# Kernel tuning notes

Measured on AMD Instinct MI355X. Metric: run time of the kernel, lower is better.

## Reference

```python
import jax, jax.numpy as jnp
import numpy as np

ROPE_BASE = 10000.0

def apply_rope(x, offset=0):
    # x: [B, H, L, Dh], traditional (interleaved-pair) RoPE
    B, H, L, Dh = x.shape
    pos = jnp.arange(L, dtype=jnp.float32) + offset            # [L]
    freqs = ROPE_BASE ** (-jnp.arange(0, Dh, 2, dtype=jnp.float32) / Dh)  # [Dh/2]
    theta = pos[:, None] * freqs[None, :]                      # [L, Dh/2]
    cos, sin = jnp.cos(theta), jnp.sin(theta)
    x1 = x[..., 0::2]                                          # [B,H,L,Dh/2]
    x2 = x[..., 1::2]
    r1 = x1 * cos - x2 * sin
    r2 = x1 * sin + x2 * cos
    return jnp.stack([r1, r2], axis=-1).reshape(B, H, L, Dh)


def setup_inputs() -> dict:
    key = jax.random.key(0)
    ks = jax.random.split(key, 5)
    B, L, D = 2, 2048, 2048
    s = 1.0 / np.sqrt(D)
    x = jax.random.normal(ks[0], (B, L, D), dtype=jnp.float32)
    # additive causal mask (0 on/below diagonal, -1e9 above)
    mask = jnp.where(jnp.tril(jnp.ones((L, L), dtype=bool)), 0.0, -1e9).astype(jnp.float32)
    Wq = jax.random.normal(ks[1], (D, D), dtype=jnp.float32) * s
    Wk = jax.random.normal(ks[2], (D, D), dtype=jnp.float32) * s
    Wv = jax.random.normal(ks[3], (D, D), dtype=jnp.float32) * s
    Wo = jax.random.normal(ks[4], (D, D), dtype=jnp.float32) * s
    return {"x": x, "mask": mask, "Wq": Wq, "Wk": Wk, "Wv": Wv, "Wo": Wo}


def reference(x, mask, Wq, Wk, Wv, Wo):
    num_heads = 16
    B, L, D = x.shape
    Dh = D // num_heads
    q = (x @ Wq.T).reshape(B, L, num_heads, Dh).transpose(0, 2, 1, 3)  # [B,H,L,Dh]
    k = (x @ Wk.T).reshape(B, L, num_heads, Dh).transpose(0, 2, 1, 3)
    v = (x @ Wv.T).reshape(B, L, num_heads, Dh).transpose(0, 2, 1, 3)
    q = apply_rope(q)
    k = apply_rope(k)
    scale = 1.0 / jnp.sqrt(jnp.float32(Dh))
    scores = jnp.einsum('bhqd,bhkd->bhqk', q * scale, k) + mask  # [B,H,L,L]
    probs = jax.nn.softmax(scores, axis=-1)
    vh = jnp.einsum('bhqk,bhkd->bhqd', probs, v)                 # [B,H,L,Dh]
    vh = vh.transpose(0, 2, 1, 3).reshape(B, L, D)
    out = vh @ Wo.T
    return out, k, v
```

## Files before the change

### kernel.cpp

```cpp
#include <hip/hip_runtime.h>

typedef __attribute__((ext_vector_type(4))) float f32x4;
typedef __attribute__((ext_vector_type(8))) __bf16 bf16x8;

__device__ __forceinline__ unsigned short f2b(float f) {
  unsigned int u = __builtin_bit_cast(unsigned int, f);
  u = (u + 0x7fffu + ((u >> 16) & 1u)) >> 16;
  return (unsigned short)u;
}
__device__ __forceinline__ float b2f(unsigned short h) {
  unsigned int u = ((unsigned int)h) << 16;
  return __builtin_bit_cast(float, u);
}
__device__ __forceinline__ void gl_lds16(const void* g, void* l) {
  __builtin_amdgcn_global_load_lds(
      (const __attribute__((address_space(1))) void*)g,
      (__attribute__((address_space(3))) void*)l, 16, 0, 0);
}

__global__ void prep_kernel(const float* __restrict__ x, unsigned short* __restrict__ xb,
                            const float* __restrict__ s0, const float* __restrict__ s1,
                            const float* __restrict__ s2, const float* __restrict__ s3,
                            unsigned short* __restrict__ d0, unsigned short* __restrict__ d1,
                            unsigned short* __restrict__ d2, unsigned short* __restrict__ d3,
                            float2* __restrict__ tab) {
  int z = blockIdx.y;
  int i = blockIdx.x * blockDim.x + threadIdx.x;
  if (z == 5) {
    if (i >= 131072) return;
    int l = i >> 6, k = i & 63;
    float freq = __builtin_amdgcn_exp2f(-(float)(2 * k) * (13.287712379549449f / 128.0f));
    float th = (float)l * freq;
    tab[i] = make_float2(cosf(th), sinf(th));
    return;
  }
  const float* src; unsigned short* dst; int n4;
  if (z == 0)      { src = x;  dst = xb; n4 = 2097152; }
  else if (z == 1) { src = s0; dst = d0; n4 = 1048576; }
  else if (z == 2) { src = s1; dst = d1; n4 = 1048576; }
  else if (z == 3) { src = s2; dst = d2; n4 = 1048576; }
  else             { src = s3; dst = d3; n4 = 1048576; }
  if (i >= n4) return;
  float4 v = ((const float4*)src)[i];
  ushort4 o;
  o.x = f2b(v.x); o.y = f2b(v.y); o.z = f2b(v.z); o.w = f2b(v.w);
  ((ushort4*)dst)[i] = o;
}

__global__ __launch_bounds__(256) void fix_kernel(unsigned short* __restrict__ qb,
                                                  unsigned short* __restrict__ kb,
                                                  float* __restrict__ kout,
                                                  const unsigned short* __restrict__ vb,
                                                  unsigned short* __restrict__ vt,
                                                  float* __restrict__ vout,
                                                  const float2* __restrict__ tab) {
  __shared__ unsigned short t[32][33];
  const float QS = 0.12751743f;
  int z = blockIdx.y;
  if (z == 2) {
    int bid = blockIdx.x;
    if (bid >= 8192) return;
    int lx = bid & 63, dy = (bid >> 6) & 3, bz = bid >> 8;
    int b = bz >> 4, h = bz & 15;
    int l0 = lx * 32, d0 = dy * 32;
    const unsigned short* src = vb + (size_t)b * 2048 * 2048 + h * 128;
    unsigned short* dst = vt + (size_t)bz * 128 * 2048;
    int tx = threadIdx.x & 31, ty = threadIdx.x >> 5;
#pragma unroll
    for (int i = 0; i < 4; ++i) {
      unsigned short u = src[(size_t)(l0 + ty + 8 * i) * 2048 + d0 + tx];
      t[ty + 8 * i][tx] = u;
      vout[((size_t)bz * 2048 + l0 + ty + 8 * i) * 128 + d0 + tx] = b2f(u);
    }
    __syncthreads();
#pragma unroll
    for (int i = 0; i < 4; ++i)
      dst[(size_t)(d0 + ty + 8 * i) * 2048 + l0 + tx] = t[tx][ty + 8 * i];
    return;
  }
  int p = blockIdx.x * blockDim.x + threadIdx.x;
  int i = p & 63;
  int tt = p >> 6;
  int h = tt & 15; tt >>= 4;
  int l = tt & 2047;
  int b = tt >> 11;
  int base = ((b * 2048 + l) * 2048) + h * 128 + 2 * i;
  unsigned short* buf = z ? kb : qb;
  float x1 = b2f(buf[base]), x2 = b2f(buf[base + 1]);
  float2 cs = tab[l * 64 + i];
  float r1 = x1 * cs.x - x2 * cs.y;
  float r2 = x1 * cs.y + x2 * cs.x;
  if (z == 1) {
    buf[base] = f2b(r1);
    buf[base + 1] = f2b(r2);
    int obase = ((b * 16 + h) * 2048 + l) * 128 + 2 * i;
    kout[obase] = r1; kout[obase + 1] = r2;
  } else {
    buf[base] = f2b(r1 * QS);
    buf[base + 1] = f2b(r2 * QS);
  }
}

template <int BM, int NBN, int OUT_F32>
__global__ __launch_bounds__(512, 2) void gemm4(const unsigned short* __restrict__ A,
                                                const unsigned short* __restrict__ W,
                                                void* __restrict__ C) {
  constexpr int K = 2048, NT = 32;
  constexpr int AH = BM / 2;
  constexpr int MF = BM / 64;
  constexpr int AQ = AH / 64;
  __shared__ unsigned short Asm[2][2][AH * 64];
  __shared__ unsigned short Bsm[2][2][128 * 64];

  const int tid = threadIdx.x, lane = tid & 63, wv = tid >> 6;
  const int wr = wv >> 2, wc = wv & 3;
  const int ln = lane & 15, kg = lane >> 4;

  const int cpx = (int)gridDim.x >> 3;
  const int swzb = ((int)blockIdx.x & 7) * cpx + ((int)blockIdx.x >> 3);
  const int bm = swzb / NBN, bn = swzb % NBN;
  const int m0 = bm * BM, n0 = bn * 256;

  const int rr = lane >> 3;
  const int sws = ((lane & 7) ^ (rr & 7)) * 8;
  const unsigned short* pA = A + (size_t)(m0 + wv * 8 * AQ + rr) * K + sws;
  const unsigned short* pB = W + (size_t)(n0 + wv * 16 + rr) * K + sws;

#define STA_(dd, hh, tt)                                                         \
  { _Pragma("unroll") for (int q = 0; q < AQ; ++q)                               \
      gl_lds16(pA + ((size_t)(hh)*AH + q * 8) * K + (size_t)(tt)*64,             \
               &Asm[dd][hh][(wv * 8 * AQ + q * 8) * 64 + lane * 8]); }
#define STB_(dd, hh, tt)                                                         \
  { _Pragma("unroll") for (int q = 0; q < 2; ++q)                                \
      gl_lds16(pB + ((size_t)(hh)*128 + q * 8) * K + (size_t)(tt)*64,            \
               &Bsm[dd][hh][(wv * 16 + q * 8) * 64 + lane * 8]); }

  const int sw0 = (kg ^ (ln & 7)) * 8;
  const int sw1 = ((4 + kg) ^ (ln & 7)) * 8;
  const int rae = (wr * (AH / 2) + ln) * 64;
  const int rbe = (wc * 32 + ln) * 64;

  f32x4 acc[2 * MF][4] = {};
  bf16x8 aA[MF][2], bB[2][2][2];

#define LDA_(dd, mh)                                                              \
  { _Pragma("unroll") for (int mf = 0; mf < MF; ++mf) {                           \
      aA[mf][0] = *(const bf16x8*)&Asm[dd][mh][rae + mf * 1024 + sw0];            \
      aA[mf][1] = *(const bf16x8*)&Asm[dd][mh][rae + mf * 1024 + sw1];            \
    } }
#define LDB_(dd, bh)                                                              \
  { _Pragma("unroll") for (int nf = 0; nf < 2; ++nf) {                            \
      bB[bh][nf][0] = *(const bf16x8*)&Bsm[dd][bh][rbe + nf * 1024 + sw0];        \
      bB[bh][nf][1] = *(const bf16x8*)&Bsm[dd][bh][rbe + nf * 1024 + sw1];        \
    } }

#define QMM(mh, bh)                                                               \
  {                                                                               \
    __builtin_amdgcn_s_setprio(1);                                                \
    _Pragma("unroll") for (int mf = 0; mf < MF; ++mf)                             \
        _Pragma("unroll") for (int nf = 0; nf < 2; ++nf) {                        \
      acc[(mh)*MF + mf][(bh)*2 + nf] = __builtin_amdgcn_mfma_f32_16x16x32_bf16(   \
          aA[mf][0], bB[bh][nf][0], acc[(mh)*MF + mf][(bh)*2 + nf], 0, 0, 0);     \
      acc[(mh)*MF + mf][(bh)*2 + nf] = __builtin_amdgcn_mfma_f32_16x16x32_bf16(   \
          aA[mf][1], bB[bh][nf][1], acc[(mh)*MF + mf][(bh)*2 + nf], 0, 0, 0);     \
    }                                                                             \
    __builtin_amdgcn_s_setprio(0);                                                \
  }

#define BAR   { __builtin_amdgcn_s_barrier(); __builtin_amdgcn_sched_barrier(0); }
#define VWAIT                                                                     \
  { if (BM == 256) { asm volatile("s_waitcnt vmcnt(4)" ::: "memory"); }           \
    else { asm volatile("s_waitcnt vmcnt(3)" ::: "memory"); } }
#define VW0   { asm volatile("s_waitcnt vmcnt(0)" ::: "memory"); }

  STA_(0, 0, 0); STB_(0, 0, 0); STB_(0, 1, 0); STA_(0, 1, 0);
  STA_(1, 0, 1); STB_(1, 1, 1);
  VWAIT;

  for (int T = 0; T < NT; T += 2) {
    const bool more = (T + 2) < NT;
    LDA_(0, 0); LDB_(0, 0);
    STB_(1, 0, T + 1);
    BAR; QMM(0, 0); BAR;
    LDB_(0, 1);
    STA_(1, 1, T + 1);
    BAR; QMM(0, 1); BAR;
    LDA_(0, 1);
    if (more) STA_(0, 0, T + 2);
    BAR; QMM(1, 1); BAR;
    if (more) { STB_(0, 1, T + 2); VWAIT; } else { VW0; }
    BAR; QMM(1, 0); BAR;
    LDA_(1, 0); LDB_(1, 0);
    if (more) STB_(0, 0, T + 2);
    BAR; QMM(0, 0); BAR;
    LDB_(1, 1);
    if (more) STA_(0, 1, T + 2);
    BAR; QMM(0, 1); BAR;
    LDA_(1, 1);
    if (more) STA_(1, 0, T + 3);
    BAR; QMM(1, 1); BAR;
    if (more) { STB_(1, 1, T + 3); VWAIT; }
    BAR; QMM(1, 0); BAR;
  }

  const int mat = bn >> 3;
  unsigned short* Cb = (unsigned short*)C;
  float* Cf = (float*)C;
#pragma unroll
  for (int mh = 0; mh < 2; ++mh)
#pragma unroll
    for (int mf = 0; mf < MF; ++mf)
#pragma unroll
      for (int j = 0; j < 4; ++j) {
        int row = m0 + mh * AH + wr * (AH / 2) + mf * 16 + kg * 4 + j;
        size_t rb = (size_t)mat * 8388608 + (size_t)row * 2048 + (size_t)((bn & 7) * 256);
#pragma unroll
        for (int bh = 0; bh < 2; ++bh)
#pragma unroll
          for (int nf = 0; nf < 2; ++nf) {
            int col = bh * 128 + wc * 32 + nf * 16 + ln;
            float v = acc[mh * MF + mf][bh * 2 + nf][j];
            if (OUT_F32) Cf[rb + col] = v;
            else Cb[rb + col] = f2b(v);
          }
      }
#undef STA_
#undef STB_
#undef LDA_
#undef LDB_
#undef QMM
#undef BAR
#undef VWAIT
#undef VW0
}

__global__ __launch_bounds__(256, 2) void attn5_kernel(const unsigned short* __restrict__ Qb,
                                                       const unsigned short* __restrict__ Kb,
                                                       const unsigned short* __restrict__ Vt,
                                                       unsigned short* __restrict__ Ob) {
  __shared__ unsigned short KS[2][8192];
  __shared__ unsigned short VS[8192];
  __shared__ unsigned short PS[4][2048];
  const int D = 2048, L = 2048;
  int tid = threadIdx.x, lane = tid & 63, w = tid >> 6;
  int ln = lane & 15, kg = lane >> 4;
  int bid = blockIdx.x;
  int g = bid >> 5, bh = bid & 31;
  int qt = (g < 8) ? (15 - g) : (g - 8);
  int b = bh >> 4, h = bh & 15;
  const size_t base = (size_t)b * L * D + h * 128;
  const unsigned short* Kp = Kb + base;
  const unsigned short* Qp = Qb + base;
  unsigned short* Op = Ob + base;
  const unsigned short* Vp = Vt + (size_t)bh * 128 * L;

  int q0 = qt * 128;
  int qw0 = q0 + w * 32;

  bf16x8 aq[2][4];
#pragma unroll
  for (int m = 0; m < 2; ++m)
#pragma unroll
    for (int kc = 0; kc < 4; ++kc)
      aq[m][kc] = *(const bf16x8*)&Qp[(size_t)(qw0 + m * 16 + ln) * D + kc * 32 + kg * 8];

  f32x4 o[2][8] = {};
  float m2[2][4], ls[2][4];
#pragma unroll
  for (int m = 0; m < 2; ++m)
#pragma unroll
    for (int j = 0; j < 4; ++j) { m2[m][j] = -1e30f; ls[m][j] = 0.f; }

  int l16 = lane >> 4, l8 = lane >> 3, l7 = lane & 7;

#define STAGE_K(T, NB)                                                                 \
  { int kv0_ = (T) << 6;                                                               \
    _Pragma("unroll") for (int i = 0; i < 4; ++i) {                                    \
      int cK = w * 4 + i;                                                              \
      int r = cK * 4 + l16;                                                            \
      int sw = ln ^ (r & 7);                                                           \
      gl_lds16(Kp + (size_t)(kv0_ + r) * D + sw * 8, &KS[NB][cK * 512 + lane * 8]); } }
#define STAGE_V(T)                                                                     \
  { int kv0_ = (T) << 6;                                                               \
    _Pragma("unroll") for (int i = 0; i < 4; ++i) {                                    \
      int cK = w * 4 + i;                                                              \
      int dh = cK * 8 + l8;                                                            \
      int sv = l7 ^ (dh & 7);                                                          \
      gl_lds16(Vp + (size_t)dh * L + kv0_ + sv * 8, &VS[cK * 512 + lane * 8]); } }

  int nt = 2 * qt + 2;
  int mask_t = 2 * qt + (w >> 1);

  STAGE_K(0, 0);
  __syncthreads();

  for (int t = 0; t < nt; ++t) {
    int cur = t & 1;
    STAGE_V(t);
    bool morek = (t + 1) < nt;
    if (morek) STAGE_K(t + 1, cur ^ 1);

    if (t <= mask_t) {
      int kv0 = t << 6;
      f32x4 s[2][4] = {};
      __builtin_amdgcn_s_setprio(1);
#pragma unroll
      for (int n = 0; n < 4; ++n)
#pragma unroll
        for (int kc = 0; kc < 4; ++kc) {
          bf16x8 bk = *(const bf16x8*)&KS[cur][(n * 16 + ln) * 128 + (((kc << 2) + kg) ^ (ln & 7)) * 8];
          s[0][n] = __builtin_amdgcn_mfma_f32_16x16x32_bf16(aq[0][kc], bk, s[0][n], 0, 0, 0);
          s[1][n] = __builtin_amdgcn_mfma_f32_16x16x32_bf16(aq[1][kc], bk, s[1][n], 0, 0, 0);
        }
      __builtin_amdgcn_s_setprio(0);
      if (t == mask_t) {
#pragma unroll
        for (int m = 0; m < 2; ++m)
#pragma unroll
          for (int n = 0; n < 4; ++n)
#pragma unroll
            for (int j = 0; j < 4; ++j)
              if (kv0 + n * 16 + ln > qw0 + m * 16 + kg * 4 + j) s[m][n][j] = -1e30f;
      }
      float pmax[2][4];
      bool near = true;
#pragma unroll
      for (int m = 0; m < 2; ++m)
#pragma unroll
        for (int j = 0; j < 4; ++j) {
          pmax[m][j] = fmaxf(fmaxf(s[m][0][j], s[m][1][j]), fmaxf(s[m][2][j], s[m][3][j]));
          near = near && (pmax[m][j] <= m2[m][j] + 8.0f);
        }
      if (!__all(near)) {
#pragma unroll
        for (int m = 0; m < 2; ++m)
#pragma unroll
          for (int j = 0; j < 4; ++j) {
            float mx = pmax[m][j];
#pragma unroll
            for (int d = 1; d < 16; d <<= 1) mx = fmaxf(mx, __shfl_xor(mx, d));
            mx = fmaxf(mx, m2[m][j]);
            float al = __builtin_amdgcn_exp2f(m2[m][j] - mx);
            m2[m][j] = mx;
            ls[m][j] *= al;
#pragma unroll
            for (int dt = 0; dt < 8; ++dt) o[m][dt][j] *= al;
          }
      }
#pragma unroll
      for (int m = 0; m < 2; ++m)
#pragma unroll
        for (int j = 0; j < 4; ++j) {
          int row = m * 16 + kg * 4 + j;
          float acc = 0.f;
#pragma unroll
          for (int n = 0; n < 4; ++n) {
            float p = __builtin_amdgcn_exp2f(s[m][n][j] - m2[m][j]);
            acc += p;
            unsigned int u = __builtin_bit_cast(unsigned int, p);
            PS[w][row * 64 + (((n * 2 + (ln >> 3)) ^ (row & 7)) * 8) + (ln & 7)] =
                (unsigned short)(u >> 16);
          }
          ls[m][j] += acc;
        }
    }

    if (morek) { asm volatile("s_waitcnt vmcnt(4)" ::: "memory"); }
    else       { asm volatile("s_waitcnt vmcnt(0)" ::: "memory"); }
    __builtin_amdgcn_s_barrier();
    __builtin_amdgcn_sched_barrier(0);

    if (t <= mask_t) {
      __builtin_amdgcn_s_setprio(1);
#pragma unroll
      for (int kst = 0; kst < 2; ++kst) {
        bf16x8 ap0 = *(const bf16x8*)&PS[w][(ln) * 64 + (((kst << 2) + kg) ^ (ln & 7)) * 8];
        bf16x8 ap1 = *(const bf16x8*)&PS[w][(16 + ln) * 64 + (((kst << 2) + kg) ^ (ln & 7)) * 8];
#pragma unroll
        for (int dt = 0; dt < 8; ++dt) {
          bf16x8 bv = *(const bf16x8*)&VS[(dt * 16 + ln) * 64 + (((kst << 2) + kg) ^ (ln & 7)) * 8];
          o[0][dt] = __builtin_amdgcn_mfma_f32_16x16x32_bf16(ap0, bv, o[0][dt], 0, 0, 0);
          o[1][dt] = __builtin_amdgcn_mfma_f32_16x16x32_bf16(ap1, bv, o[1][dt], 0, 0, 0);
        }
      }
      __builtin_amdgcn_s_setprio(0);
    }
    __syncthreads();
  }
#undef STAGE_K
#undef STAGE_V

#pragma unroll
  for (int m = 0; m < 2; ++m)
#pragma unroll
    for (int j = 0; j < 4; ++j) {
      float tsum = ls[m][j];
#pragma unroll
      for (int d = 1; d < 16; d <<= 1) tsum += __shfl_xor(tsum, d);
      float inv = 1.0f / tsum;
      int row = qw0 + m * 16 + kg * 4 + j;
#pragma unroll
      for (int dt = 0; dt < 8; ++dt)
        Op[(size_t)row * D + dt * 16 + ln] = f2b(o[m][dt][j] * inv);
    }
}

extern "C" void kernel_launch(void* const* d_in, const int* in_sizes, int n_in,
                              void* d_out, int out_size, void* d_ws, size_t ws_size,
                              hipStream_t stream) {
  const float* x  = (const float*)d_in[0];
  const float* Wq = (const float*)d_in[2];
  const float* Wk = (const float*)d_in[3];
  const float* Wv = (const float*)d_in[4];
  const float* Wo = (const float*)d_in[5];

  char* ws = (char*)d_ws;
  unsigned short* xb  = (unsigned short*)(ws + 0);
  unsigned short* wqb = (unsigned short*)(ws + 16777216);
  unsigned short* wkb = (unsigned short*)(ws + 25165824);
  unsigned short* wvb = (unsigned short*)(ws + 33554432);
  unsigned short* wob = (unsigned short*)(ws + 41943040);
  unsigned short* qb  = (unsigned short*)(ws + 50331648);
  unsigned short* kb  = (unsigned short*)(ws + 67108864);
  unsigned short* vb  = (unsigned short*)(ws + 83886080);
  float2* tab         = (float2*)(ws + 100663296);
  unsigned short* vt  = wqb;
  unsigned short* ob  = xb;

  float* out  = (float*)d_out;
  float* kout = out + 8388608;
  float* vout = out + 16777216;

  prep_kernel<<<dim3(8192, 6), 256, 0, stream>>>(x, xb, Wq, Wk, Wv, Wo, wqb, wkb, wvb, wob, tab);

  gemm4<256, 24, 0><<<384, 512, 0, stream>>>(xb, wqb, qb);

  fix_kernel<<<dim3(16384, 3), 256, 0, stream>>>(qb, kb, kout, vb, vt, vout, tab);

  attn5_kernel<<<512, 256, 0, stream>>>(qb, kb, vt, ob);

  gemm4<128, 8, 1><<<256, 512, 0, stream>>>(ob, wob, out);
}
```

Before: 294.8 us.

## Add gemm6 with 32-wide K tiles and finer-grained load/MFMA interleave for QKV

Introduces a new GEMM kernel that halves the K tile from 64 to 32 (64 iterations instead of 32) and interleaves global-to-LDS loads with quarter-tile MFMA groups separated by barriers and vmcnt waits. It replaces gemm4 for the fused QKV projection. The aim is to shrink the LDS footprint and overlap memory traffic with compute more tightly. The cost is many more barriers per K step, which may add sync overhead.

Measured after the change: 308.2 us. +4.5%, slower.

```diff
diff --git a/kernel.cpp b/kernel.cpp
--- a/kernel.cpp
+++ b/kernel.cpp
@@ -99,6 +99,125 @@
     buf[base] = f2b(r1 * QS);
     buf[base + 1] = f2b(r2 * QS);
   }
+}
+
+template <int BM, int NBN, int OUT_F32>
+__global__ __launch_bounds__(512, 2) void gemm6(const unsigned short* __restrict__ A,
+                                                const unsigned short* __restrict__ W,
+                                                void* __restrict__ C) {
+  constexpr int K = 2048, NT = 64;
+  constexpr int AH = BM / 2;
+  constexpr int MF = BM / 64;
+  __shared__ unsigned short Asm[2][2][AH * 32];
+  __shared__ unsigned short Bsm[2][2][128 * 32];
+
+  const int tid = threadIdx.x, lane = tid & 63, wv = tid >> 6;
+  const int wr = wv >> 2, wc = wv & 3;
+  const int ln = lane & 15, kg = lane >> 4;
+
+  const int cpx = (int)gridDim.x >> 3;
+  const int swzb = ((int)blockIdx.x & 7) * cpx + ((int)blockIdx.x >> 3);
+  const int bm = swzb / NBN, bn = swzb % NBN;
+  const int m0 = bm * BM, n0 = bn * 256;
+
+  const int trow = tid >> 2;
+  const int sws = ((tid & 3) ^ (trow & 3)) * 8;
+  const unsigned short* pA = A + (size_t)(m0 + trow) * K + sws;
+  const unsigned short* pB = W + (size_t)(n0 + trow) * K + sws;
+  const int ldst = trow * 32 + (tid & 3) * 8;
+
+#define STA6(dd, hh, tt)                                                          \
+  gl_lds16(pA + (size_t)(hh) * 128 * K + (size_t)(tt) * 32, &Asm[dd][hh][ldst]);
+#define STB6(dd, hh, tt)                                                          \
+  gl_lds16(pB + (size_t)(hh) * 128 * K + (size_t)(tt) * 32, &Bsm[dd][hh][ldst]);
+
+  const int sw0 = (kg ^ (ln & 3)) * 8;
+  const int rae = (wr * 64 + ln) * 32;
+  const int rbe = (wc * 32 + ln) * 32;
+
+  f32x4 acc[2 * MF][4] = {};
+  bf16x8 aA[MF], bB[2][2];
+
+#define LDA6(dd, mh)                                                              \
+  { _Pragma("unroll") for (int mf = 0; mf < MF; ++mf)                             \
+      aA[mf] = *(const bf16x8*)&Asm[dd][mh][rae + mf * 512 + sw0]; }
+#define LDB6(dd, bh)                                                              \
+  { _Pragma("unroll") for (int nf = 0; nf < 2; ++nf)                              \
+      bB[bh][nf] = *(const bf16x8*)&Bsm[dd][bh][rbe + nf * 512 + sw0]; }
+
+#define QMM6(mh, bh)                                                              \
+  {                                                                               \
+    __builtin_amdgcn_s_setprio(1);                                                \
+    _Pragma("unroll") for (int mf = 0; mf < MF; ++mf)                             \
+        _Pragma("unroll") for (int nf = 0; nf < 2; ++nf)                          \
+      acc[(mh)*MF + mf][(bh)*2 + nf] = __builtin_amdgcn_mfma_f32_16x16x32_bf16(   \
+          aA[mf], bB[bh][nf], acc[(mh)*MF + mf][(bh)*2 + nf], 0, 0, 0);           \
+    __builtin_amdgcn_s_setprio(0);                                                \
+  }
+
+#define BAR6   { __builtin_amdgcn_s_barrier(); __builtin_amdgcn_sched_barrier(0); }
+#define VW2    { asm volatile("s_waitcnt vmcnt(2)" ::: "memory"); }
+#define VZ0    { asm volatile("s_waitcnt vmcnt(0)" ::: "memory"); }
+
+  STA6(0, 0, 0); STB6(0, 0, 0); STB6(0, 1, 0); STA6(0, 1, 0);
+  STA6(1, 0, 1); STB6(1, 1, 1);
+  VW2;
+
+  for (int T = 0; T < NT; T += 2) {
+    const bool more = (T + 2) < NT;
+    LDA6(0, 0); LDB6(0, 0);
+    STB6(1, 0, T + 1);
+    BAR6; QMM6(0, 0); BAR6;
+    LDB6(0, 1);
+    STA6(1, 1, T + 1);
+    BAR6; QMM6(0, 1); BAR6;
+    LDA6(0, 1);
+    if (more) STA6(0, 0, T + 2);
+    BAR6; QMM6(1, 1); BAR6;
+    if (more) { STB6(0, 1, T + 2); VW2; } else { VZ0; }
+    BAR6; QMM6(1, 0); BAR6;
+    LDA6(1, 0); LDB6(1, 0);
+    if (more) STB6(0, 0, T + 2);
+    BAR6; QMM6(0, 0); BAR6;
+    LDB6(1, 1);
+    if (more) STA6(0, 1, T + 2);
+    BAR6; QMM6(0, 1); BAR6;
+    LDA6(1, 1);
+    if (more) STA6(1, 0, T + 3);
+    BAR6; QMM6(1, 1); BAR6;
+    if (more) { STB6(1, 1, T + 3); VW2; }
+    BAR6; QMM6(1, 0); BAR6;
+  }
+
+  const int mat = bn >> 3;
+  unsigned short* Cb = (unsigned short*)C;
+  float* Cf = (float*)C;
+#pragma unroll
+  for (int mh = 0; mh < 2; ++mh)
+#pragma unroll
+    for (int mf = 0; mf < MF; ++mf)
+#pragma unroll
+      for (int j = 0; j < 4; ++j) {
+        int row = m0 + mh * AH + wr * 64 + mf * 16 + kg * 4 + j;
+        size_t rb = (size_t)mat * 8388608 + (size_t)row * 2048 + (size_t)((bn & 7) * 256);
+#pragma unroll
+        for (int bh = 0; bh < 2; ++bh)
+#pragma unroll
+          for (int nf = 0; nf < 2; ++nf) {
+            int col = bh * 128 + wc * 32 + nf * 16 + ln;
+            float v = acc[mh * MF + mf][bh * 2 + nf][j];
+            if (OUT_F32) Cf[rb + col] = v;
+            else Cb[rb + col] = f2b(v);
+          }
+      }
+#undef STA6
+#undef STB6
+#undef LDA6
+#undef LDB6
+#undef QMM6
+#undef BAR6
+#undef VW2
+#undef VZ0
 }
 
 template <int BM, int NBN, int OUT_F32>
@@ -433,7 +552,7 @@
 
   prep_kernel<<<dim3(8192, 6), 256, 0, stream>>>(x, xb, Wq, Wk, Wv, Wo, wqb, wkb, wvb, wob, tab);
 
-  gemm4<256, 24, 0><<<384, 512, 0, stream>>>(xb, wqb, qb);
+  gemm6<256, 24, 0><<<384, 512, 0, stream>>>(xb, wqb, qb);
 
   fix_kernel<<<dim3(16384, 3), 256, 0, stream>>>(qb, kb, kout, vb, vt, vout, tab);
 
```
